# Kernel optimization log

Hardware: AMD Instinct MI355X
Metric: run time of the kernel (lower is better)

## Reference

```python
import jax, jax.numpy as jnp
import numpy as np

NUM_HEADS = 8


def conv2x2_s2(x, w, b):
    # x: [B,C,H,W], w: [O,I,2,2], stride 2, no padding (torch Conv2d k=2,s=2)
    y = jax.lax.conv_general_dilated(
        x, w, window_strides=(2, 2), padding='VALID',
        dimension_numbers=('NCHW', 'OIHW', 'NCHW'))
    return y + b[None, :, None, None]


def up2(x):
    return jnp.repeat(jnp.repeat(x, 2, axis=2), 2, axis=3)


def setup_inputs() -> dict:
    key = jax.random.key(0)
    B, C, H, W = 1, 128, 64, 64
    N = H * W
    ks = jax.random.split(key, 7)
    p = lambda k, shape: jax.random.normal(k, shape, jnp.float32) * 0.02
    return {
        'x': jax.random.normal(ks[0], (B, N, C), jnp.float32),
        'conv1_w': p(ks[1], (C, C, 2, 2)),
        'conv1_b': jnp.zeros((C,), jnp.float32),
        'conv2_w': p(ks[2], (C, C, 2, 2)),
        'conv2_b': jnp.zeros((C,), jnp.float32),
        'q_w': p(ks[3], (C, C)),
        'kv_w': p(ks[4], (2 * C, C)),
        'proj_w': p(ks[5], (C, C)),
        'proj_b': jnp.zeros((C,), jnp.float32),
        'H': H,
        'W': W,
    }


def reference(x, conv1_w, conv1_b, conv2_w, conv2_b, q_w, kv_w, proj_w, proj_b, H, W):
    B, N, C = x.shape
    hd = C // NUM_HEADS
    scale = hd ** -0.5
    # tokens -> feature map
    x_ = x.transpose(0, 2, 1).reshape(B, C, H, W)
    # ChannelPriorQueries: conv(s2) -> up2 -> conv(s2) -> up2 (HxW preserved)
    tq = up2(conv2x2_s2(up2(conv2x2_s2(x_, conv1_w, conv1_b)), conv2_w, conv2_b))
    tq = tq.reshape(B, C, N).transpose(0, 2, 1)  # [B,N,C]
    # projections (torch Linear: y = x @ W.T)
    q = (tq @ q_w.T).reshape(B, N, NUM_HEADS, hd).transpose(0, 2, 1, 3)   # [B,h,N,d]
    kv = (x @ kv_w.T).reshape(B, N, 2, NUM_HEADS, hd).transpose(2, 0, 3, 1, 4)
    k, v = kv[0], kv[1]  # [B,h,N,d]
    # sr_ratio == 1: F.interpolate(q, size=(N, d)) is the identity
    attn = jax.nn.softmax(jnp.einsum('bhqd,bhkd->bhqk', q, k) * scale, axis=-1)
    out = jnp.einsum('bhqk,bhkd->bhqd', attn, v)
    out = out.transpose(0, 2, 1, 3).reshape(B, N, C)
    return out @ proj_w.T + proj_b
```

## Files before the change

kernel.cpp:

```cpp
#include <hip/hip_runtime.h>
#include <hip/hip_bf16.h>

#define CCH 128
#define NTOK 4096
#define NP 1024
#define NH 8
#define HD 16

typedef __attribute__((ext_vector_type(8)))  short s8v;
typedef __attribute__((ext_vector_type(16))) float f32x16;

#define OFF_Y1T   0
#define OFF_M     131072
#define OFF_QB    147456
#define OFF_AT16  147584
#define OFF_K16   180352
#define OFF_VT16  442496

__device__ inline unsigned short f2bf(float v) {
    __hip_bfloat16 b = __float2bfloat16(v);
    return *reinterpret_cast<unsigned short*>(&b);
}
__device__ inline unsigned int pk2bf(float a, float b) {
    __hip_bfloat162 t = __float22bfloat162_rn(make_float2(a, b));
    return *reinterpret_cast<unsigned int*>(&t);
}
__device__ inline int crow_of(int r, int hi) { return (r & 3) + 8*(r >> 2) + 4*hi; }

union BU { unsigned int u[4]; s8v v; };

__global__ void __launch_bounds__(256) kA_prep(const float* __restrict__ x,
        const float* __restrict__ w1, const float* __restrict__ b1,
        const float* __restrict__ w2, const float* __restrict__ b2,
        const float* __restrict__ qw, const float* __restrict__ kvw,
        float* __restrict__ ws,
        unsigned short* __restrict__ k16, unsigned short* __restrict__ vt16) {
    __shared__ float smem[2048];
    const int b = blockIdx.x;
    const int tid = threadIdx.x;
    const int w = tid >> 6, lane = tid & 63;
    const int ql = lane & 31, hi = lane >> 5;

    if (b < 256) {
        const int n0 = (b >> 1) * 32;
        const int octile = (b & 1) * 4 + w;
        const int oc0 = octile * 32;
        const bool isK = (octile < 4);
        const float* arow = (isK ? x + (n0 + ql)*CCH : kvw + (oc0 + ql)*CCH) + hi*8;
        const float* brow = (isK ? kvw + (oc0 + ql)*CCH : x + (n0 + ql)*CCH) + hi*8;
        f32x16 acc = {};
        float4 a0 = *reinterpret_cast<const float4*>(arow);
        float4 a1 = *reinterpret_cast<const float4*>(arow + 4);
        float4 b0 = *reinterpret_cast<const float4*>(brow);
        float4 b1v = *reinterpret_cast<const float4*>(brow + 4);
        for (int kk = 0; kk < 8; ++kk) {
            float4 na0 = a0, na1 = a1, nb0 = b0, nb1 = b1v;
            if (kk < 7) {
                na0 = *reinterpret_cast<const float4*>(arow + (kk+1)*16);
                na1 = *reinterpret_cast<const float4*>(arow + (kk+1)*16 + 4);
                nb0 = *reinterpret_cast<const float4*>(brow + (kk+1)*16);
                nb1 = *reinterpret_cast<const float4*>(brow + (kk+1)*16 + 4);
            }
            BU au, bu;
            au.u[0] = pk2bf(a0.x, a0.y); au.u[1] = pk2bf(a0.z, a0.w);
            au.u[2] = pk2bf(a1.x, a1.y); au.u[3] = pk2bf(a1.z, a1.w);
            bu.u[0] = pk2bf(b0.x, b0.y); bu.u[1] = pk2bf(b0.z, b0.w);
            bu.u[2] = pk2bf(b1v.x, b1v.y); bu.u[3] = pk2bf(b1v.z, b1v.w);
            acc = __builtin_amdgcn_mfma_f32_32x32x16_bf16(au.v, bu.v, acc, 0, 0, 0);
            a0 = na0; a1 = na1; b0 = nb0; b1v = nb1;
        }
        if (isK) {
            const int oc = oc0 + ql, h = oc >> 4, d = oc & 15;
            #pragma unroll
            for (int r = 0; r < 16; ++r) {
                const int n = n0 + crow_of(r, hi);
                k16[(h*NTOK + n)*HD + d] = f2bf(acc[r]);
            }
        } else {
            #pragma unroll
            for (int r = 0; r < 16; ++r) {
                const int oc = oc0 + crow_of(r, hi);
                vt16[(oc - CCH)*NTOK + n0 + ql] = f2bf(acc[r]);
            }
        }
    } else if (b < 512) {
        const int pp = tid >> 7, o = tid & 127;
        float* xs = smem + pp * 1024;
        const int p0 = (b - 256) * 4 + pp * 2;
        #pragma unroll
        for (int pl = 0; pl < 2; ++pl) {
            int p = p0 + pl;
            int i = p >> 5, j = p & 31;
            int t00 = (2*i)*64 + 2*j;
            float4 v;
            v.x = x[(t00     )*CCH + o];
            v.y = x[(t00 +  1)*CCH + o];
            v.z = x[(t00 + 64)*CCH + o];
            v.w = x[(t00 + 65)*CCH + o];
            *reinterpret_cast<float4*>(&xs[(pl*CCH + o)*4]) = v;
        }
        __syncthreads();
        float acc0 = 0.f, acc1 = 0.f;
        #pragma unroll 8
        for (int c = 0; c < CCH; ++c) {
            float4 w4 = *reinterpret_cast<const float4*>(&w1[(o*CCH + c)*4]);
            float4 a  = *reinterpret_cast<const float4*>(&xs[c*4]);
            float4 bq = *reinterpret_cast<const float4*>(&xs[(CCH + c)*4]);
            acc0 += w4.x*a.x + w4.y*a.y + w4.z*a.z + w4.w*a.w;
            acc1 += w4.x*bq.x + w4.y*bq.y + w4.z*bq.z + w4.w*bq.w;
        }
        ws[OFF_Y1T + (p0+0)*CCH + o] = acc0 + b1[o];
        ws[OFF_Y1T + (p0+1)*CCH + o] = acc1 + b1[o];
    } else {
        int id = (b - 512) * 256 + tid;
        int r = id >> 7, c = id & 127;
        const float* qr = qw + r*CCH;
        float acc = 0.f;
        #pragma unroll 4
        for (int o4 = 0; o4 < 32; ++o4) {
            float4 q4 = *reinterpret_cast<const float4*>(qr + o4*4);
            float4 wa = *reinterpret_cast<const float4*>(&w2[((o4*4+0)*CCH + c)*4]);
            float4 wb = *reinterpret_cast<const float4*>(&w2[((o4*4+1)*CCH + c)*4]);
            float4 wc = *reinterpret_cast<const float4*>(&w2[((o4*4+2)*CCH + c)*4]);
            float4 wd = *reinterpret_cast<const float4*>(&w2[((o4*4+3)*CCH + c)*4]);
            acc += q4.x*(wa.x+wa.y+wa.z+wa.w);
            acc += q4.y*(wb.x+wb.y+wb.z+wb.w);
            acc += q4.z*(wc.x+wc.y+wc.z+wc.w);
            acc += q4.w*(wd.x+wd.y+wd.z+wd.w);
        }
        ws[OFF_M + id] = acc * 0.25f;
        if (id < CCH) {
            float a = 0.f;
            #pragma unroll 8
            for (int o = 0; o < CCH; ++o) a += qw[id*CCH + o] * b2[o];
            ws[OFF_QB + id] = a * 0.25f;
        }
    }
}

__global__ void __launch_bounds__(1024) kB_attn(const float* __restrict__ ws,
                                                const unsigned short* __restrict__ k16,
                                                const unsigned short* __restrict__ vt16,
                                                unsigned short* __restrict__ at16) {
    __shared__ float ys[32*CCH];
    __shared__ unsigned short qs[32*24];
    __shared__ float oacc[16*HD*32];
    __shared__ float lbuf[16*32];
    const int tid = threadIdx.x;
    const int h = blockIdx.x >> 5, qt = blockIdx.x & 31;

    reinterpret_cast<float4*>(ys)[tid] =
        reinterpret_cast<const float4*>(ws + OFF_Y1T + qt*32*CCH)[tid];
    __syncthreads();

    {
        const int qq = tid >> 5, r = (tid >> 1) & 15, half = tid & 1;
        const float* Mr = ws + OFF_M + (h*HD + r)*CCH + half*64;
        const float* yr = ys + qq*CCH + half*64;
        float a = 0.f;
        #pragma unroll
        for (int c4 = 0; c4 < 16; ++c4) {
            float4 m4 = *reinterpret_cast<const float4*>(Mr + c4*4);
            float4 y4 = *reinterpret_cast<const float4*>(yr + c4*4);
            a += m4.x*y4.x + m4.y*y4.y + m4.z*y4.z + m4.w*y4.w;
        }
        a += __shfl_xor(a, 1);
        if (half == 0) qs[qq*24 + r] = f2bf(a + ws[OFF_QB + h*HD + r]);
    }
    __syncthreads();

    const int s = tid >> 6;
    const int lane = tid & 63;
    const int ql = lane & 31;
    const int hi = lane >> 5;

    s8v qf = *reinterpret_cast<const s8v*>(qs + ql*24 + hi*8);

    const unsigned short* kp = k16 + (h*NTOK)*HD;
    const unsigned short* vp = vt16 + (h*HD + ql)*NTOK;
    const bool vvalid = (ql < HD);

    f32x16 acc = {};
    float lsum = 0.f;

    const int kbase = s*256;
    s8v kf = *reinterpret_cast<const s8v*>(kp + (kbase + ql)*HD + hi*8);
    s8v vf1 = {}, vf2 = {};
    if (vvalid) {
        vf1 = *reinterpret_cast<const s8v*>(vp + kbase + hi*8);
        vf2 = *reinterpret_cast<const s8v*>(vp + kbase + 16 + hi*8);
    }

    for (int c = 0; c < 8; ++c) {
        s8v kf_n = kf, vf1_n = vf1, vf2_n = vf2;
        if (c < 7) {
            const int kb2 = kbase + (c+1)*32;
            kf_n = *reinterpret_cast<const s8v*>(kp + (kb2 + ql)*HD + hi*8);
            if (vvalid) {
                vf1_n = *reinterpret_cast<const s8v*>(vp + kb2 + hi*8);
                vf2_n = *reinterpret_cast<const s8v*>(vp + kb2 + 16 + hi*8);
            }
        }

        f32x16 z = {};
        f32x16 st = __builtin_amdgcn_mfma_f32_32x32x16_bf16(kf, qf, z, 0, 0, 0);

        float p[16];
        #pragma unroll
        for (int r = 0; r < 16; ++r) p[r] = __expf(st[r]);
        float t0 = (p[0]+p[1]) + (p[2]+p[3]);
        float t1 = (p[4]+p[5]) + (p[6]+p[7]);
        float t2 = (p[8]+p[9]) + (p[10]+p[11]);
        float t3 = (p[12]+p[13]) + (p[14]+p[15]);
        lsum += (t0 + t1) + (t2 + t3);

        unsigned int W[8];
        #pragma unroll
        for (int i = 0; i < 8; ++i) W[i] = pk2bf(p[2*i], p[2*i+1]);

        BU b1x, b2x;
        {
            unsigned int s0 = (unsigned int)__shfl_xor((int)W[0], 32);
            unsigned int s1 = (unsigned int)__shfl_xor((int)W[1], 32);
            unsigned int s2 = (unsigned int)__shfl_xor((int)W[2], 32);
            unsigned int s3 = (unsigned int)__shfl_xor((int)W[3], 32);
            b1x.u[0] = hi ? s2 : W[0];
            b1x.u[1] = hi ? s3 : W[1];
            b1x.u[2] = hi ? W[2] : s0;
            b1x.u[3] = hi ? W[3] : s1;
            unsigned int s4 = (unsigned int)__shfl_xor((int)W[4], 32);
            unsigned int s5 = (unsigned int)__shfl_xor((int)W[5], 32);
            unsigned int s6 = (unsigned int)__shfl_xor((int)W[6], 32);
            unsigned int s7 = (unsigned int)__shfl_xor((int)W[7], 32);
            b2x.u[0] = hi ? s6 : W[4];
            b2x.u[1] = hi ? s7 : W[5];
            b2x.u[2] = hi ? W[6] : s4;
            b2x.u[3] = hi ? W[7] : s5;
        }

        acc = __builtin_amdgcn_mfma_f32_32x32x16_bf16(vf1, b1x.v, acc, 0, 0, 0);
        acc = __builtin_amdgcn_mfma_f32_32x32x16_bf16(vf2, b2x.v, acc, 0, 0, 0);

        kf = kf_n; vf1 = vf1_n; vf2 = vf2_n;
    }

    float lt = lsum + __shfl_xor(lsum, 32);
    if (lane < 32) lbuf[s*32 + ql] = lt;
    #pragma unroll
    for (int r = 0; r < 8; ++r) {
        int d = crow_of(r, hi);
        oacc[(s*HD + d)*32 + ql] = acc[r];
    }
    __syncthreads();

    if (tid < 512) {
        const int q2 = tid & 31, d2 = tid >> 5;
        float ltot = 0.f, o = 0.f;
        #pragma unroll
        for (int ss = 0; ss < 16; ++ss) {
            ltot += lbuf[ss*32 + q2];
            o    += oacc[(ss*HD + d2)*32 + q2];
        }
        at16[(qt*32 + q2)*CCH + h*HD + d2] = f2bf(o / ltot);
    }
}

__global__ void __launch_bounds__(256) k5_proj(const unsigned short* __restrict__ at16,
                                               const float* __restrict__ pw,
                                               const float* __restrict__ pb,
                                               float* __restrict__ out) {
    const int ptile = blockIdx.x;
    const int w = threadIdx.x >> 6, lane = threadIdx.x & 63;
    const int ql = lane & 31, hi = lane >> 5;
    const int oc0 = w * 32;
    const unsigned short* arow = at16 + (ptile*32 + ql)*CCH + hi*8;
    const float* brow = pw + (oc0 + ql)*CCH + hi*8;

    f32x16 acc = {};
    s8v af = *reinterpret_cast<const s8v*>(arow);
    float4 b0 = *reinterpret_cast<const float4*>(brow);
    float4 b1v = *reinterpret_cast<const float4*>(brow + 4);
    for (int kk = 0; kk < 8; ++kk) {
        s8v naf = af; float4 nb0 = b0, nb1 = b1v;
        if (kk < 7) {
            naf = *reinterpret_cast<const s8v*>(arow + (kk+1)*16);
            nb0 = *reinterpret_cast<const float4*>(brow + (kk+1)*16);
            nb1 = *reinterpret_cast<const float4*>(brow + (kk+1)*16 + 4);
        }
        BU bu;
        bu.u[0] = pk2bf(b0.x, b0.y); bu.u[1] = pk2bf(b0.z, b0.w);
        bu.u[2] = pk2bf(b1v.x, b1v.y); bu.u[3] = pk2bf(b1v.z, b1v.w);
        acc = __builtin_amdgcn_mfma_f32_32x32x16_bf16(af, bu.v, acc, 0, 0, 0);
        af = naf; b0 = nb0; b1v = nb1;
    }

    const float bias = pb[oc0 + ql];
    #pragma unroll
    for (int r = 0; r < 16; ++r) {
        const int j = crow_of(r, hi);
        const int t00 = 128*ptile + 2*j;
        const float v = acc[r] + bias;
        out[(t00     )*CCH + oc0 + ql] = v;
        out[(t00 +  1)*CCH + oc0 + ql] = v;
        out[(t00 + 64)*CCH + oc0 + ql] = v;
        out[(t00 + 65)*CCH + oc0 + ql] = v;
    }
}

extern "C" void kernel_launch(void* const* d_in, const int* in_sizes, int n_in,
                              void* d_out, int out_size, void* d_ws, size_t ws_size,
                              hipStream_t stream) {
    const float* x   = (const float*)d_in[0];
    const float* w1  = (const float*)d_in[1];
    const float* b1  = (const float*)d_in[2];
    const float* w2  = (const float*)d_in[3];
    const float* b2  = (const float*)d_in[4];
    const float* qw  = (const float*)d_in[5];
    const float* kvw = (const float*)d_in[6];
    const float* pw  = (const float*)d_in[7];
    const float* pb  = (const float*)d_in[8];
    float* ws  = (float*)d_ws;
    float* out = (float*)d_out;

    unsigned short* at16 = (unsigned short*)(ws + OFF_AT16);
    unsigned short* k16  = (unsigned short*)(ws + OFF_K16);
    unsigned short* vt16 = (unsigned short*)(ws + OFF_VT16);

    hipLaunchKernelGGL(kA_prep, dim3(576), dim3(256), 0, stream,
                       x, w1, b1, w2, b2, qw, kvw, ws, k16, vt16);
    hipLaunchKernelGGL(kB_attn, dim3(256), dim3(1024), 0, stream,
                       ws, k16, vt16, at16);
    hipLaunchKernelGGL(k5_proj, dim3(32), dim3(256), 0, stream, at16, pw, pb, out);
}
```

Baseline: 53.33 us.

## Fuse output projection into attention kernel via last-block atomic counter

Removes the separate projection kernel launch. Each attention block increments a per-query-tile counter, and the last of the eight head blocks for that tile runs the MFMA projection and writes the upsampled output. The counters are zeroed in the prep kernel. This saves one launch and its gap, at the cost of a serialized tail in the last-finishing blocks plus atomic and fence overhead.

```diff
diff --git a/kernel.cpp b/kernel.cpp
--- a/kernel.cpp
+++ b/kernel.cpp
@@ -16,6 +16,7 @@
 #define OFF_AT16  147584
 #define OFF_K16   180352
 #define OFF_VT16  442496
+#define OFF_CNT   704640
 
 __device__ inline unsigned short f2bf(float v) {
     __hip_bfloat16 b = __float2bfloat16(v);
@@ -112,6 +113,8 @@
         ws[OFF_Y1T + (p0+0)*CCH + o] = acc0 + b1[o];
         ws[OFF_Y1T + (p0+1)*CCH + o] = acc1 + b1[o];
     } else {
+        if (b == 512 && tid < 32)
+            ((unsigned*)(ws + OFF_CNT))[tid] = 0u;
         int id = (b - 512) * 256 + tid;
         int r = id >> 7, c = id & 127;
         const float* qr = qw + r*CCH;
@@ -141,11 +144,16 @@
 __global__ void __launch_bounds__(1024) kB_attn(const float* __restrict__ ws,
                                                 const unsigned short* __restrict__ k16,
                                                 const unsigned short* __restrict__ vt16,
-                                                unsigned short* __restrict__ at16) {
+                                                unsigned short* __restrict__ at16,
+                                                unsigned* __restrict__ cnt,
+                                                const float* __restrict__ pw,
+                                                const float* __restrict__ pb,
+                                                float* __restrict__ out) {
     __shared__ float ys[32*CCH];
     __shared__ unsigned short qs[32*24];
     __shared__ float oacc[16*HD*32];
     __shared__ float lbuf[16*32];
+    __shared__ unsigned wonFlag;
     const int tid = threadIdx.x;
     const int h = blockIdx.x >> 5, qt = blockIdx.x & 31;
 
@@ -263,47 +271,53 @@
         }
         at16[(qt*32 + q2)*CCH + h*HD + d2] = f2bf(o / ltot);
     }
-}
-
-__global__ void __launch_bounds__(256) k5_proj(const unsigned short* __restrict__ at16,
-                                               const float* __restrict__ pw,
-                                               const float* __restrict__ pb,
-                                               float* __restrict__ out) {
-    const int ptile = blockIdx.x;
-    const int w = threadIdx.x >> 6, lane = threadIdx.x & 63;
-    const int ql = lane & 31, hi = lane >> 5;
-    const int oc0 = w * 32;
-    const unsigned short* arow = at16 + (ptile*32 + ql)*CCH + hi*8;
-    const float* brow = pw + (oc0 + ql)*CCH + hi*8;
-
-    f32x16 acc = {};
-    s8v af = *reinterpret_cast<const s8v*>(arow);
-    float4 b0 = *reinterpret_cast<const float4*>(brow);
-    float4 b1v = *reinterpret_cast<const float4*>(brow + 4);
-    for (int kk = 0; kk < 8; ++kk) {
-        s8v naf = af; float4 nb0 = b0, nb1 = b1v;
-        if (kk < 7) {
-            naf = *reinterpret_cast<const s8v*>(arow + (kk+1)*16);
-            nb0 = *reinterpret_cast<const float4*>(brow + (kk+1)*16);
-            nb1 = *reinterpret_cast<const float4*>(brow + (kk+1)*16 + 4);
-        }
-        BU bu;
-        bu.u[0] = pk2bf(b0.x, b0.y); bu.u[1] = pk2bf(b0.z, b0.w);
-        bu.u[2] = pk2bf(b1v.x, b1v.y); bu.u[3] = pk2bf(b1v.z, b1v.w);
-        acc = __builtin_amdgcn_mfma_f32_32x32x16_bf16(af, bu.v, acc, 0, 0, 0);
-        af = naf; b0 = nb0; b1v = nb1;
-    }
-
-    const float bias = pb[oc0 + ql];
-    #pragma unroll
-    for (int r = 0; r < 16; ++r) {
-        const int j = crow_of(r, hi);
-        const int t00 = 128*ptile + 2*j;
-        const float v = acc[r] + bias;
-        out[(t00     )*CCH + oc0 + ql] = v;
-        out[(t00 +  1)*CCH + oc0 + ql] = v;
-        out[(t00 + 64)*CCH + oc0 + ql] = v;
-        out[(t00 + 65)*CCH + oc0 + ql] = v;
+
+    __syncthreads();
+    if (tid == 0) {
+        __threadfence();
+        unsigned old = __hip_atomic_fetch_add(&cnt[qt], 1u,
+                        __ATOMIC_ACQ_REL, __HIP_MEMORY_SCOPE_AGENT);
+        wonFlag = (old == NH - 1) ? 1u : 0u;
+    }
+    __syncthreads();
+    if (wonFlag && tid < 256) {
+        __threadfence();
+        const int ptile = qt;
+        const int w = tid >> 6, lane2 = tid & 63;
+        const int ql2 = lane2 & 31, hi2 = lane2 >> 5;
+        const int oc0 = w * 32;
+        const unsigned short* arow = at16 + (ptile*32 + ql2)*CCH + hi2*8;
+        const float* brow = pw + (oc0 + ql2)*CCH + hi2*8;
+
+        f32x16 pacc = {};
+        s8v af = *reinterpret_cast<const s8v*>(arow);
+        float4 b0 = *reinterpret_cast<const float4*>(brow);
+        float4 b1v = *reinterpret_cast<const float4*>(brow + 4);
+        for (int kk = 0; kk < 8; ++kk) {
+            s8v naf = af; float4 nb0 = b0, nb1 = b1v;
+            if (kk < 7) {
+                naf = *reinterpret_cast<const s8v*>(arow + (kk+1)*16);
+                nb0 = *reinterpret_cast<const float4*>(brow + (kk+1)*16);
+                nb1 = *reinterpret_cast<const float4*>(brow + (kk+1)*16 + 4);
+            }
+            BU bu;
+            bu.u[0] = pk2bf(b0.x, b0.y); bu.u[1] = pk2bf(b0.z, b0.w);
+            bu.u[2] = pk2bf(b1v.x, b1v.y); bu.u[3] = pk2bf(b1v.z, b1v.w);
+            pacc = __builtin_amdgcn_mfma_f32_32x32x16_bf16(af, bu.v, pacc, 0, 0, 0);
+            af = naf; b0 = nb0; b1v = nb1;
+        }
+
+        const float bias = pb[oc0 + ql2];
+        #pragma unroll
+        for (int r = 0; r < 16; ++r) {
+            const int j = crow_of(r, hi2);
+            const int t00 = 128*ptile + 2*j;
+            const float v = pacc[r] + bias;
+            out[(t00     )*CCH + oc0 + ql2] = v;
+            out[(t00 +  1)*CCH + oc0 + ql2] = v;
+            out[(t00 + 64)*CCH + oc0 + ql2] = v;
+            out[(t00 + 65)*CCH + oc0 + ql2] = v;
+        }
     }
 }
 
@@ -325,10 +339,10 @@
     unsigned short* at16 = (unsigned short*)(ws + OFF_AT16);
     unsigned short* k16  = (unsigned short*)(ws + OFF_K16);
     unsigned short* vt16 = (unsigned short*)(ws + OFF_VT16);
+    unsigned* cnt = (unsigned*)(ws + OFF_CNT);
 
     hipLaunchKernelGGL(kA_prep, dim3(576), dim3(256), 0, stream,
                        x, w1, b1, w2, b2, qw, kvw, ws, k16, vt16);
     hipLaunchKernelGGL(kB_attn, dim3(256), dim3(1024), 0, stream,
-                       ws, k16, vt16, at16);
-    hipLaunchKernelGGL(k5_proj, dim3(32), dim3(256), 0, stream, at16, pw, pb, out);
-}
+                       ws, k16, vt16, at16, cnt, pw, pb, out);
+}
```

Result: slower. 67.80 us (+27.1%).
